# Optimization experiments

Hardware: AMD Instinct MI355X
Metric: run time of the kernel (lower is better)

Reference implementation:

```python
import jax, jax.numpy as jnp
import numpy as np

OUT = 7           # pooled output size
SR = 2            # sampling_ratio
SCALES = (0.25, 0.125, 0.0625, 0.03125)
K_MIN = 2         # -log2(scales[0])
CANON_SCALE = 224.0
CANON_LVL = 4.0
EPS = 1e-6


def map_levels(boxes):
    # boxes: [N,4] in image coords -> level index in [0, 3]
    area = (boxes[:, 2] - boxes[:, 0]) * (boxes[:, 3] - boxes[:, 1])
    s = jnp.sqrt(area)
    lvl = jnp.floor(CANON_LVL + jnp.log2(s / CANON_SCALE + EPS))
    lvl = jnp.clip(lvl, K_MIN, K_MIN + len(SCALES) - 1)
    return lvl.astype(jnp.int32) - K_MIN


def _sample_coords(lo, bin_sz):
    # sample points within each of OUT bins, SR samples per bin -> [OUT*SR]
    grid = (jnp.arange(OUT, dtype=jnp.float32)[:, None] * bin_sz
            + (jnp.arange(SR, dtype=jnp.float32)[None, :] + 0.5) * bin_sz / SR)
    return lo + grid.reshape(-1)


def _roi_align_single(feat, img, box, scale):
    # feat: [B,C,H,W] (closed over batch under vmap), img: scalar int, box: [4]
    H, W = feat.shape[2], feat.shape[3]
    x1 = box[0] * scale
    y1 = box[1] * scale
    x2 = box[2] * scale
    y2 = box[3] * scale
    roi_w = jnp.maximum(x2 - x1, 1.0)
    roi_h = jnp.maximum(y2 - y1, 1.0)
    ys = _sample_coords(y1, roi_h / OUT)  # [14]
    xs = _sample_coords(x1, roi_w / OUT)  # [14]
    P = OUT * SR
    yg = jnp.broadcast_to(ys[:, None], (P, P)).reshape(-1)  # [196]
    xg = jnp.broadcast_to(xs[None, :], (P, P)).reshape(-1)  # [196]
    # ROIAlign CUDA semantics: out-of-range samples contribute 0
    valid = (yg >= -1.0) & (yg <= H) & (xg >= -1.0) & (xg <= W)
    y = jnp.clip(yg, 0.0, H - 1)
    x = jnp.clip(xg, 0.0, W - 1)
    y0 = jnp.floor(y).astype(jnp.int32)
    x0 = jnp.floor(x).astype(jnp.int32)
    y1i = jnp.minimum(y0 + 1, H - 1)
    x1i = jnp.minimum(x0 + 1, W - 1)
    ly = y - y0
    lx = x - x0
    hy = 1.0 - ly
    hx = 1.0 - lx
    # advanced indices (img, y, x) separated by ':' slice -> result [196, C]
    v00 = feat[img, :, y0, x0]
    v01 = feat[img, :, y0, x1i]
    v10 = feat[img, :, y1i, x0]
    v11 = feat[img, :, y1i, x1i]
    val = ((hy * hx)[:, None] * v00 + (hy * lx)[:, None] * v01
           + (ly * hx)[:, None] * v10 + (ly * lx)[:, None] * v11)
    val = jnp.where(valid[:, None], val, 0.0)
    # [196,C] -> [OUT,SR,OUT,SR,C] -> average over sampling grid -> [OUT,OUT,C]
    val = val.reshape(OUT, SR, OUT, SR, -1).mean(axis=(1, 3))
    return jnp.transpose(val, (2, 0, 1))  # [C,7,7]


def _pooler(feats, boxes, img_ids):
    levels = map_levels(boxes)  # [N]
    N = boxes.shape[0]
    C = feats[0].shape[1]
    result = jnp.zeros((N, C, OUT, OUT), dtype=feats[0].dtype)
    roi_align = jax.vmap(_roi_align_single, in_axes=(None, 0, 0, None))
    for lvl, (feat, scale) in enumerate(zip(feats, SCALES)):
        out_l = roi_align(feat, img_ids, boxes, scale)  # [N,C,7,7]
        result = jnp.where((levels == lvl)[:, None, None, None], out_l, result)
    return result


def setup_inputs() -> dict:
    key = jax.random.key(0)
    ks = jax.random.split(key, 7)
    B, C, N = 2, 256, 1000
    feat0 = jax.random.normal(ks[0], (B, C, 200, 200), jnp.float32)
    feat1 = jax.random.normal(ks[1], (B, C, 100, 100), jnp.float32)
    feat2 = jax.random.normal(ks[2], (B, C, 50, 50), jnp.float32)
    feat3 = jax.random.normal(ks[3], (B, C, 25, 25), jnp.float32)
    # log-uniform box sizes in [16, 400] px spread ROIs across all 4 levels
    wh = jnp.exp(jax.random.uniform(ks[4], (N, 2), minval=jnp.log(16.0),
                                    maxval=jnp.log(400.0)))
    xy = jax.random.uniform(ks[5], (N, 2)) * (800.0 - wh)
    boxes = jnp.concatenate([xy, xy + wh], axis=1)  # [N,4] x1,y1,x2,y2
    img_ids = jax.random.randint(ks[6], (N,), 0, B, dtype=jnp.int32)
    return {"feat0": feat0, "feat1": feat1, "feat2": feat2, "feat3": feat3,
            "boxes": boxes, "img_ids": img_ids}


def reference(feat0, feat1, feat2, feat3, boxes, img_ids):
    return _pooler((feat0, feat1, feat2, feat3), boxes, img_ids)
```

## Files before the change

kernel.cpp:

```cpp
#include <hip/hip_runtime.h>
#include <hip/hip_fp16.h>

#define OUTD 7
#define PD 14
#define NCH 256

#define TOFF0 0
#define TOFF1 20480000
#define TOFF2 25600000
#define TOFF3 26880000
#define TTOT  27200000
#define TBASE_BYTES 16384

__global__ __launch_bounds__(1024)
void sort_kernel(const float* __restrict__ boxes,
                 const int*   __restrict__ img_ids,
                 int* __restrict__ order, int N)
{
    __shared__ unsigned long long kv[1024];
    const int t = threadIdx.x;

    unsigned int key = 0xFFFFFFFFu;
    if (t < N) {
        const float bx1 = boxes[t * 4 + 0];
        const float by1 = boxes[t * 4 + 1];
        const float bx2 = boxes[t * 4 + 2];
        const float by2 = boxes[t * 4 + 3];
        const float area = (bx2 - bx1) * (by2 - by1);
        const float s = sqrtf(area);
        float lvlf = floorf(4.0f + log2f(s / 224.0f + 1e-6f));
        lvlf = fminf(fmaxf(lvlf, 2.0f), 5.0f);
        const int lvl = (int)lvlf - 2;
        const float scales[4] = {0.25f, 0.125f, 0.0625f, 0.03125f};
        const float sc = scales[lvl];
        int cx = (int)(0.5f * (bx1 + bx2) * sc);
        int cy = (int)(0.5f * (by1 + by2) * sc);
        cx = min(max(cx, 0), 127);
        cy = min(max(cy, 0), 127);
        unsigned int m = 0;
#pragma unroll
        for (int b = 0; b < 7; ++b)
            m |= ((cy >> b) & 1u) << (2 * b + 1) | ((cx >> b) & 1u) << (2 * b);
        key = ((((unsigned)lvl << 1) | (unsigned)img_ids[t]) << 14) | m;
    }
    kv[t] = ((unsigned long long)key << 32) | (unsigned)t;
    __syncthreads();

    for (int k = 2; k <= 1024; k <<= 1) {
        for (int j = k >> 1; j > 0; j >>= 1) {
            const int ixj = t ^ j;
            if (ixj > t) {
                const bool up = ((t & k) == 0);
                const unsigned long long a = kv[t], b = kv[ixj];
                if ((a > b) == up) { kv[t] = b; kv[ixj] = a; }
            }
            __syncthreads();
        }
    }
    if (t < N) order[t] = (int)(kv[t] & 0xFFFFFFFFu);
}

__global__ __launch_bounds__(512)
void transpose_kernel(const float* __restrict__ f0, const float* __restrict__ f1,
                      const float* __restrict__ f2, const float* __restrict__ f3,
                      __half* __restrict__ T)
{
    const int t = threadIdx.x;
    int id = blockIdx.x;
    const int img = (id >= 832) ? 1 : 0; if (img) id -= 832;
    int lvl, pt;
    if (id < 625)      { lvl = 0; pt = id; }
    else if (id < 782) { lvl = 1; pt = id - 625; }
    else if (id < 822) { lvl = 2; pt = id - 782; }
    else               { lvl = 3; pt = id - 822; }

    const int  Ps[4]   = {40000, 10000, 2500, 625};
    const long TO[4]   = {TOFF0, TOFF1, TOFF2, TOFF3};
    const float* feats[4] = {f0, f1, f2, f3};
    const int P = Ps[lvl];
    const float* __restrict__ src = feats[lvl] + (size_t)img * NCH * (size_t)P;
    __half* __restrict__ dst = T + TO[lvl] + (size_t)img * (size_t)P * NCH;
    const int p0 = pt * 64;

    __shared__ float tile[64][260];

    const int a  = t & 15;
    const int cg = t >> 4;
    const int p4 = a * 4;

#pragma unroll
    for (int i = 0; i < 8; ++i) {
        const int cs = cg + 32 * i;
        const float* sp = src + (size_t)cs * P + p0;
        float4 v;
        if (((P & 3) == 0) && (p0 + p4 + 3 < P)) {
            v = *(const float4*)(sp + p4);
        } else {
            const int m = P - 1 - p0;
            v.x = sp[min(p4 + 0, m)]; v.y = sp[min(p4 + 1, m)];
            v.z = sp[min(p4 + 2, m)]; v.w = sp[min(p4 + 3, m)];
        }
        tile[p4 + 0][cs] = v.x;
        tile[p4 + 1][cs] = v.y;
        tile[p4 + 2][cs] = v.z;
        tile[p4 + 3][cs] = v.w;
    }
    __syncthreads();

    const int c4 = (t & 63) * 4;
    const int w  = t >> 6;
#pragma unroll
    for (int i = 0; i < 8; ++i) {
        const int p = w + 8 * i;
        if (p0 + p < P) {
            const __half2 h0 = __floats2half2_rn(tile[p][c4 + 0], tile[p][c4 + 1]);
            const __half2 h1 = __floats2half2_rn(tile[p][c4 + 2], tile[p][c4 + 3]);
            uint2 o;
            o.x = *(const unsigned int*)&h0;
            o.y = *(const unsigned int*)&h1;
            *(uint2*)(dst + (size_t)(p0 + p) * NCH + c4) = o;
        }
    }
}

__global__ __launch_bounds__(256)
void pooler_t_kernel(const __half* __restrict__ T,
                     const float* __restrict__ boxes,
                     const int*   __restrict__ img_ids,
                     const int*   __restrict__ order,
                     float* __restrict__ out, int N)
{
    int bx = blockIdx.x;
    int sidx;
    if ((N & 7) == 0) sidx = (bx & 7) * (N >> 3) + (bx >> 3);
    else              sidx = bx;
    const int roi = order[sidx];
    const int t = threadIdx.x;

    const float bx1 = boxes[roi * 4 + 0];
    const float by1 = boxes[roi * 4 + 1];
    const float bx2 = boxes[roi * 4 + 2];
    const float by2 = boxes[roi * 4 + 3];

    const float area = (bx2 - bx1) * (by2 - by1);
    const float s    = sqrtf(area);
    float lvlf = floorf(4.0f + log2f(s / 224.0f + 1e-6f));
    lvlf = fminf(fmaxf(lvlf, 2.0f), 5.0f);
    const int lvl = (int)lvlf - 2;

    const float scales[4] = {0.25f, 0.125f, 0.0625f, 0.03125f};
    const int   dims[4]   = {200, 100, 50, 25};
    const int   Ps[4]     = {40000, 10000, 2500, 625};
    const long  TO[4]     = {TOFF0, TOFF1, TOFF2, TOFF3};

    const float scale = scales[lvl];
    const int H = dims[lvl];
    const int W = H;
    const int img = img_ids[roi];
    const __half* __restrict__ tb = T + TO[lvl] + (size_t)img * (size_t)Ps[lvl] * NCH;

    const float x1 = bx1 * scale, y1 = by1 * scale;
    const float x2 = bx2 * scale, y2 = by2 * scale;
    const float roi_w = fmaxf(x2 - x1, 1.0f);
    const float roi_h = fmaxf(y2 - y1, 1.0f);
    const float bw = roi_w / (float)OUTD;
    const float bh = roi_h / (float)OUTD;

    __shared__ float4 s_yt[PD];
    __shared__ float4 s_xt[PD];
    __shared__ float  s_out[49 * 260];

    if (t < PD) {
        const int i = t >> 1, j = t & 1;
        const float yg = y1 + (float)i * bh + ((float)j + 0.5f) * bh * 0.5f;
        const float v = ((yg >= -1.0f) && (yg <= (float)H)) ? 1.0f : 0.0f;
        const float y = fminf(fmaxf(yg, 0.0f), (float)(H - 1));
        const int y0 = (int)floorf(y);
        const int y1i = min(y0 + 1, H - 1);
        const float ly = y - (float)y0;
        float4 r;
        r.x = __int_as_float(y0 * W);
        r.y = __int_as_float(y1i * W);
        r.z = (1.0f - ly) * v;
        r.w = ly * v;
        s_yt[t] = r;
    } else if (t < 2 * PD) {
        const int tt = t - PD;
        const int i = tt >> 1, j = tt & 1;
        const float xg = x1 + (float)i * bw + ((float)j + 0.5f) * bw * 0.5f;
        const float v = ((xg >= -1.0f) && (xg <= (float)W)) ? 1.0f : 0.0f;
        const float x = fminf(fmaxf(xg, 0.0f), (float)(W - 1));
        const int x0 = (int)floorf(x);
        const int x1i = min(x0 + 1, W - 1);
        const float lx = x - (float)x0;
        float4 r;
        r.x = __int_as_float(x0);
        r.y = __int_as_float(x1i);
        r.z = (1.0f - lx) * v;
        r.w = lx * v;
        s_xt[tt] = r;
    }
    __syncthreads();

    const int lane = t & 63;
    const int w    = t >> 6;
    const int c4   = lane * 4;

    for (int bin = w; bin < 49; bin += 4) {
        const int ph = (bin * 37) >> 8;
        const int pw = bin - ph * 7;
        float4 acc = {0.0f, 0.0f, 0.0f, 0.0f};
#pragma unroll
        for (int sy = 0; sy < 2; ++sy) {
            const float4 yt = s_yt[ph * 2 + sy];
            const int r0 = __float_as_int(yt.x);
            const int r1 = __float_as_int(yt.y);
            const float hy = yt.z, ly = yt.w;
#pragma unroll
            for (int sx = 0; sx < 2; ++sx) {
                const float4 xt = s_xt[pw * 2 + sx];
                const int xa = __float_as_int(xt.x);
                const int xb = __float_as_int(xt.y);
                const float hx = xt.z, lx = xt.w;
                const float w00 = hy * hx, w01 = hy * lx, w10 = ly * hx, w11 = ly * lx;

                const uint2 q00 = *(const uint2*)(tb + ((size_t)(r0 + xa) << 8) + c4);
                const uint2 q01 = *(const uint2*)(tb + ((size_t)(r0 + xb) << 8) + c4);
                const uint2 q10 = *(const uint2*)(tb + ((size_t)(r1 + xa) << 8) + c4);
                const uint2 q11 = *(const uint2*)(tb + ((size_t)(r1 + xb) << 8) + c4);

                const float2 a0 = __half22float2(*(const __half2*)&q00.x);
                const float2 a1 = __half22float2(*(const __half2*)&q00.y);
                const float2 b0 = __half22float2(*(const __half2*)&q01.x);
                const float2 b1 = __half22float2(*(const __half2*)&q01.y);
                const float2 c0 = __half22float2(*(const __half2*)&q10.x);
                const float2 c1 = __half22float2(*(const __half2*)&q10.y);
                const float2 d0 = __half22float2(*(const __half2*)&q11.x);
                const float2 d1 = __half22float2(*(const __half2*)&q11.y);

                acc.x += w00 * a0.x + w01 * b0.x + w10 * c0.x + w11 * d0.x;
                acc.y += w00 * a0.y + w01 * b0.y + w10 * c0.y + w11 * d0.y;
                acc.z += w00 * a1.x + w01 * b1.x + w10 * c1.x + w11 * d1.x;
                acc.w += w00 * a1.y + w01 * b1.y + w10 * c1.y + w11 * d1.y;
            }
        }
        float4 r;
        r.x = acc.x * 0.25f; r.y = acc.y * 0.25f;
        r.z = acc.z * 0.25f; r.w = acc.w * 0.25f;
        *(float4*)(&s_out[bin * 260 + c4]) = r;
    }
    __syncthreads();

    float* __restrict__ outbase = out + (size_t)roi * (NCH * 49);
#pragma unroll
    for (int i = 0; i < 49; ++i) {
        const int e = t + i * 256;
        const int c = (int)(((unsigned)e * 21400u) >> 20);
        const int bin = e - c * 49;
        outbase[e] = s_out[bin * 260 + c];
    }
}

#define LCHUNK 32
__global__ __launch_bounds__(256)
void pooler_legacy(const float* __restrict__ f0,
                   const float* __restrict__ f1,
                   const float* __restrict__ f2,
                   const float* __restrict__ f3,
                   const float* __restrict__ boxes,
                   const int*   __restrict__ img_ids,
                   const int*   __restrict__ order,
                   float* __restrict__ out, int N)
{
    int bx = blockIdx.x;
    int sidx;
    if ((N & 7) == 0) sidx = (bx & 7) * (N >> 3) + (bx >> 3);
    else              sidx = bx;
    const int roi = order[sidx];

    const int c0  = blockIdx.y * LCHUNK;
    const int t   = threadIdx.x;

    const float bx1 = boxes[roi * 4 + 0];
    const float by1 = boxes[roi * 4 + 1];
    const float bx2 = boxes[roi * 4 + 2];
    const float by2 = boxes[roi * 4 + 3];

    const float area = (bx2 - bx1) * (by2 - by1);
    const float s    = sqrtf(area);
    float lvlf = floorf(4.0f + log2f(s / 224.0f + 1e-6f));
    lvlf = fminf(fmaxf(lvlf, 2.0f), 5.0f);
    const int lvl = (int)lvlf - 2;

    const float scales[4] = {0.25f, 0.125f, 0.0625f, 0.03125f};
    const int   dims[4]   = {200, 100, 50, 25};
    const float* feats[4] = {f0, f1, f2, f3};

    const float scale = scales[lvl];
    const int H = dims[lvl];
    const int W = H;
    const int plane = H * W;

    const int img = img_ids[roi];
    const float* __restrict__ base0 =
        feats[lvl] + (size_t)img * NCH * (size_t)plane + (size_t)c0 * plane;

    const float x1 = bx1 * scale, y1 = by1 * scale;
    const float x2 = bx2 * scale, y2 = by2 * scale;
    const float roi_w = fmaxf(x2 - x1, 1.0f);
    const float roi_h = fmaxf(y2 - y1, 1.0f);
    const float bw = roi_w / (float)OUTD;
    const float bh = roi_h / (float)OUTD;

    __shared__ float4 s_yt[PD];
    __shared__ float4 s_xt[PD];
    __shared__ float4 s_xw[OUTD];
    __shared__ int    s_xf[OUTD];
    __shared__ int    s_ok[OUTD];

    if (t < PD) {
        const int i = t >> 1, j = t & 1;
        const float yg = y1 + (float)i * bh + ((float)j + 0.5f) * bh * 0.5f;
        const float v = ((yg >= -1.0f) && (yg <= (float)H)) ? 1.0f : 0.0f;
        const float y = fminf(fmaxf(yg, 0.0f), (float)(H - 1));
        const int y0 = (int)floorf(y);
        const int y1i = min(y0 + 1, H - 1);
        const float ly = y - (float)y0;
        float4 r;
        r.x = __int_as_float(y0 * W);
        r.y = __int_as_float(y1i * W);
        r.z = (1.0f - ly) * v;
        r.w = ly * v;
        s_yt[t] = r;
    } else if (t < 2 * PD) {
        const int tt = t - PD;
        const int i = tt >> 1, j = tt & 1;
        const float xg = x1 + (float)i * bw + ((float)j + 0.5f) * bw * 0.5f;
        const float v = ((xg >= -1.0f) && (xg <= (float)W)) ? 1.0f : 0.0f;
        const float x = fminf(fmaxf(xg, 0.0f), (float)(W - 1));
        const int x0 = (int)floorf(x);
        const float lx = x - (float)x0;
        const float hx = 1.0f - lx;
        const int edge = (x0 == W - 1);
        float4 r;
        r.x = __int_as_float(min(x0, W - 2));
        r.y = edge ? 0.0f   : hx * v;
        r.z = edge ? hx * v : lx * v;
        r.w = 0.0f;
        s_xt[tt] = r;
    } else if (t < 2 * PD + OUTD) {
        const int pw = t - 2 * PD;
        float w[4] = {0.0f, 0.0f, 0.0f, 0.0f};
        int ca[2], cb[2];
        float hxv[2], lxv[2];
#pragma unroll
        for (int j = 0; j < 2; ++j) {
            const float xg = x1 + (float)pw * bw + ((float)j + 0.5f) * bw * 0.5f;
            const float v = ((xg >= -1.0f) && (xg <= (float)W)) ? 1.0f : 0.0f;
            const float x = fminf(fmaxf(xg, 0.0f), (float)(W - 1));
            const int x0 = (int)floorf(x);
            const float lx = x - (float)x0;
            ca[j] = x0;
            cb[j] = min(x0 + 1, W - 1);
            hxv[j] = (1.0f - lx) * v;
            lxv[j] = lx * v;
        }
        const int ok = (cb[1] - ca[0]) <= 3;
        int xf = min(ca[0], W - 4);
        if (xf < 0) xf = 0;
        w[(ca[0] - xf) & 3] += hxv[0];
        w[(cb[0] - xf) & 3] += lxv[0];
        w[(ca[1] - xf) & 3] += hxv[1];
        w[(cb[1] - xf) & 3] += lxv[1];
        float4 wv; wv.x = w[0]; wv.y = w[1]; wv.z = w[2]; wv.w = w[3];
        s_xw[pw] = wv;
        s_xf[pw] = xf;
        s_ok[pw] = ok;
    }
    __syncthreads();

    const bool fused = s_ok[0] && s_ok[1] && s_ok[2] && s_ok[3] &&
                       s_ok[4] && s_ok[5] && s_ok[6];

    float* __restrict__ outbase = out + ((size_t)roi * NCH + c0) * 49;

    if (fused) {
        auto g4 = [&](const float* __restrict__ fp, int ph, int pw, float4* P) {
            const float4 yt0 = s_yt[2 * ph];
            const float4 yt1 = s_yt[2 * ph + 1];
            const int xf = s_xf[pw];
            P[0] = *(const float4*)(fp + __float_as_int(yt0.x) + xf);
            P[1] = *(const float4*)(fp + __float_as_int(yt0.y) + xf);
            P[2] = *(const float4*)(fp + __float_as_int(yt1.x) + xf);
            P[3] = *(const float4*)(fp + __float_as_int(yt1.y) + xf);
        };
        auto r4 = [&](int ph, int pw, const float4* P) -> float {
            const float4 w   = s_xw[pw];
            const float4 yt0 = s_yt[2 * ph];
            const float4 yt1 = s_yt[2 * ph + 1];
            const float d0 = w.x * P[0].x + w.y * P[0].y + w.z * P[0].z + w.w * P[0].w;
            const float d1 = w.x * P[1].x + w.y * P[1].y + w.z * P[1].z + w.w * P[1].w;
            const float d2 = w.x * P[2].x + w.y * P[2].y + w.z * P[2].z + w.w * P[2].w;
            const float d3 = w.x * P[3].x + w.y * P[3].y + w.z * P[3].z + w.w * P[3].w;
            return yt0.z * d0 + yt0.w * d1 + yt1.z * d2 + yt1.w * d3;
        };
        {
            int eA[4], phA[4], pwA[4];
            const float* fpA[4];
#pragma unroll
            for (int j = 0; j < 4; ++j) {
                const int e = t + j * 256;
                const int c = e / 49, bin = e - c * 49;
                phA[j] = bin / 7;
                pwA[j] = bin - phA[j] * 7;
                eA[j]  = e;
                fpA[j] = base0 + (size_t)c * plane;
            }
            float4 P[4][4];
#pragma unroll
            for (int j = 0; j < 4; ++j) g4(fpA[j], phA[j], pwA[j], P[j]);
            __builtin_amdgcn_sched_barrier(0);
#pragma unroll
            for (int j = 0; j < 4; ++j)
                outbase[eA[j]] = r4(phA[j], pwA[j], P[j]) * 0.25f;
        }
        {
            int eA[2], phA[2], pwA[2];
            const float* fpA[2];
#pragma unroll
            for (int j = 0; j < 2; ++j) {
                const int e = t + (4 + j) * 256;
                const int c = e / 49, bin = e - c * 49;
                phA[j] = bin / 7;
                pwA[j] = bin - phA[j] * 7;
                eA[j]  = e;
                fpA[j] = base0 + (size_t)c * plane;
            }
            float4 P[2][4];
#pragma unroll
            for (int j = 0; j < 2; ++j) g4(fpA[j], phA[j], pwA[j], P[j]);
            __builtin_amdgcn_sched_barrier(0);
#pragma unroll
            for (int j = 0; j < 2; ++j)
                outbase[eA[j]] = r4(phA[j], pwA[j], P[j]) * 0.25f;
        }
        if (t < 32) {
            const int e = 1536 + t;
            const int c = e / 49, bin = e - c * 49;
            const int ph = bin / 7, pw = bin - ph * 7;
            const float* fp = base0 + (size_t)c * plane;
            float4 P[4];
            g4(fp, ph, pw, P);
            outbase[e] = r4(ph, pw, P) * 0.25f;
        }
    } else {
        auto gather = [&](const float* __restrict__ fp, int ph, int pw, float2* P) {
#pragma unroll
            for (int sy = 0; sy < 2; ++sy) {
                const float4 yt = s_yt[ph * 2 + sy];
                const int ro0 = __float_as_int(yt.x);
                const int ro1 = __float_as_int(yt.y);
#pragma unroll
                for (int sx = 0; sx < 2; ++sx) {
                    const float4 xt = s_xt[pw * 2 + sx];
                    const int xa = __float_as_int(xt.x);
                    P[(sy * 2 + sx) * 2 + 0] = *(const float2*)(fp + ro0 + xa);
                    P[(sy * 2 + sx) * 2 + 1] = *(const float2*)(fp + ro1 + xa);
                }
            }
        };
        auto reduce = [&](int ph, int pw, const float2* P) -> float {
            float acc = 0.0f;
#pragma unroll
            for (int sy = 0; sy < 2; ++sy) {
                const float4 yt = s_yt[ph * 2 + sy];
                const float hy = yt.z, ly = yt.w;
#pragma unroll
                for (int sx = 0; sx < 2; ++sx) {
                    const float4 xt = s_xt[pw * 2 + sx];
                    const float wlo = xt.y, whi = xt.z;
                    const float2 p0 = P[(sy * 2 + sx) * 2 + 0];
                    const float2 p1 = P[(sy * 2 + sx) * 2 + 1];
                    acc += hy * (wlo * p0.x + whi * p0.y)
                         + ly * (wlo * p1.x + whi * p1.y);
                }
            }
            return acc;
        };
#pragma unroll
        for (int kk = 0; kk < 2; ++kk) {
            int eA[3], phA[3], pwA[3];
            const float* fpA[3];
#pragma unroll
            for (int j = 0; j < 3; ++j) {
                const int e = t + (kk * 3 + j) * 256;
                const int c = e / 49, bin = e - c * 49;
                phA[j] = bin / 7;
                pwA[j] = bin - phA[j] * 7;
                eA[j]  = e;
                fpA[j] = base0 + (size_t)c * plane;
            }
            float2 P[3][8];
#pragma unroll
            for (int j = 0; j < 3; ++j) gather(fpA[j], phA[j], pwA[j], P[j]);
            __builtin_amdgcn_sched_barrier(0);
#pragma unroll
            for (int j = 0; j < 3; ++j)
                outbase[eA[j]] = reduce(phA[j], pwA[j], P[j]) * 0.25f;
        }
        if (t < 32) {
            const int e = 1536 + t;
            const int c = e / 49, bin = e - c * 49;
            const int ph = bin / 7, pw = bin - ph * 7;
            const float* fp = base0 + (size_t)c * plane;
            float2 P[8];
            gather(fp, ph, pw, P);
            outbase[e] = reduce(ph, pw, P) * 0.25f;
        }
    }
}

extern "C" void kernel_launch(void* const* d_in, const int* in_sizes, int n_in,
                              void* d_out, int out_size, void* d_ws, size_t ws_size,
                              hipStream_t stream) {
    const float* f0    = (const float*)d_in[0];
    const float* f1    = (const float*)d_in[1];
    const float* f2    = (const float*)d_in[2];
    const float* f3    = (const float*)d_in[3];
    const float* boxes = (const float*)d_in[4];
    const int*   ids   = (const int*)d_in[5];
    float* out = (float*)d_out;
    int*   order = (int*)d_ws;

    const int N = in_sizes[4] / 4;

    const size_t need = (size_t)TBASE_BYTES + (size_t)TTOT * sizeof(__half);

    sort_kernel<<<1, 1024, 0, stream>>>(boxes, ids, order, N);

    if (ws_size >= need) {
        __half* T = (__half*)((char*)d_ws + TBASE_BYTES);
        transpose_kernel<<<1664, 512, 0, stream>>>(f0, f1, f2, f3, T);
        pooler_t_kernel<<<N, 256, 0, stream>>>(T, boxes, ids, order, out, N);
    } else {
        dim3 grid(N, NCH / LCHUNK);
        pooler_legacy<<<grid, 256, 0, stream>>>(f0, f1, f2, f3, boxes, ids, order, out, N);
    }
}
```

Measured before the change: 217.6 us.

## Fuse ROI sort into transpose kernel and halve transpose tile size

The separate single-block sort launch is folded into the transpose kernel as an extra block, so the sort runs alongside the feature transpose instead of as its own serialized launch. The transpose tile shrinks from 64 to 32 positions with 256-thread blocks, doubling the block count and cutting shared memory per block, which is meant to raise occupancy. The sort block now handles 1024 elements with 256 threads in strided loops. The fast path is limited to N of at most 1024.

After: 232.2 us. 1.07x slower.

```diff
diff --git a/kernel.cpp b/kernel.cpp
--- a/kernel.cpp
+++ b/kernel.cpp
@@ -12,20 +12,18 @@
 #define TTOT  27200000
 #define TBASE_BYTES 16384
 
-__global__ __launch_bounds__(1024)
-void sort_kernel(const float* __restrict__ boxes,
-                 const int*   __restrict__ img_ids,
-                 int* __restrict__ order, int N)
+#define NTILES_IMG 1662
+#define NB_TRANS   3324
+
+__device__ __forceinline__ unsigned int roi_key(const float* boxes,
+                                                const int* img_ids, int e, int N)
 {
-    __shared__ unsigned long long kv[1024];
-    const int t = threadIdx.x;
-
     unsigned int key = 0xFFFFFFFFu;
-    if (t < N) {
-        const float bx1 = boxes[t * 4 + 0];
-        const float by1 = boxes[t * 4 + 1];
-        const float bx2 = boxes[t * 4 + 2];
-        const float by2 = boxes[t * 4 + 3];
+    if (e < N) {
+        const float bx1 = boxes[e * 4 + 0];
+        const float by1 = boxes[e * 4 + 1];
+        const float bx2 = boxes[e * 4 + 2];
+        const float by2 = boxes[e * 4 + 3];
         const float area = (bx2 - bx1) * (by2 - by1);
         const float s = sqrtf(area);
         float lvlf = floorf(4.0f + log2f(s / 224.0f + 1e-6f));
@@ -41,38 +39,53 @@
 #pragma unroll
         for (int b = 0; b < 7; ++b)
             m |= ((cy >> b) & 1u) << (2 * b + 1) | ((cx >> b) & 1u) << (2 * b);
-        key = ((((unsigned)lvl << 1) | (unsigned)img_ids[t]) << 14) | m;
-    }
-    kv[t] = ((unsigned long long)key << 32) | (unsigned)t;
-    __syncthreads();
-
-    for (int k = 2; k <= 1024; k <<= 1) {
-        for (int j = k >> 1; j > 0; j >>= 1) {
-            const int ixj = t ^ j;
-            if (ixj > t) {
-                const bool up = ((t & k) == 0);
-                const unsigned long long a = kv[t], b = kv[ixj];
-                if ((a > b) == up) { kv[t] = b; kv[ixj] = a; }
-            }
-            __syncthreads();
-        }
-    }
-    if (t < N) order[t] = (int)(kv[t] & 0xFFFFFFFFu);
+        key = ((((unsigned)lvl << 1) | (unsigned)img_ids[e]) << 14) | m;
+    }
+    return key;
 }
 
-__global__ __launch_bounds__(512)
-void transpose_kernel(const float* __restrict__ f0, const float* __restrict__ f1,
-                      const float* __restrict__ f2, const float* __restrict__ f3,
-                      __half* __restrict__ T)
+__global__ __launch_bounds__(256)
+void prep_kernel(const float* __restrict__ f0, const float* __restrict__ f1,
+                 const float* __restrict__ f2, const float* __restrict__ f3,
+                 const float* __restrict__ boxes,
+                 const int*   __restrict__ img_ids,
+                 int* __restrict__ order,
+                 __half* __restrict__ T, int N)
 {
+    __shared__ __align__(16) float smbuf[32 * 260];
     const int t = threadIdx.x;
+
+    if (blockIdx.x == NB_TRANS) {
+        unsigned long long* kv = (unsigned long long*)smbuf;
+        for (int e = t; e < 1024; e += 256)
+            kv[e] = ((unsigned long long)roi_key(boxes, img_ids, e, N) << 32)
+                    | (unsigned)e;
+        __syncthreads();
+        for (int k = 2; k <= 1024; k <<= 1) {
+            for (int j = k >> 1; j > 0; j >>= 1) {
+                for (int i = t; i < 1024; i += 256) {
+                    const int ixj = i ^ j;
+                    if (ixj > i) {
+                        const bool up = ((i & k) == 0);
+                        const unsigned long long a = kv[i], b = kv[ixj];
+                        if ((a > b) == up) { kv[i] = b; kv[ixj] = a; }
+                    }
+                }
+                __syncthreads();
+            }
+        }
+        for (int e = t; e < 1024; e += 256)
+            if (e < N) order[e] = (int)(kv[e] & 0xFFFFFFFFu);
+        return;
+    }
+
     int id = blockIdx.x;
-    const int img = (id >= 832) ? 1 : 0; if (img) id -= 832;
+    const int img = (id >= NTILES_IMG) ? 1 : 0; if (img) id -= NTILES_IMG;
     int lvl, pt;
-    if (id < 625)      { lvl = 0; pt = id; }
-    else if (id < 782) { lvl = 1; pt = id - 625; }
-    else if (id < 822) { lvl = 2; pt = id - 782; }
-    else               { lvl = 3; pt = id - 822; }
+    if (id < 1250)      { lvl = 0; pt = id; }
+    else if (id < 1563) { lvl = 1; pt = id - 1250; }
+    else if (id < 1642) { lvl = 2; pt = id - 1563; }
+    else                { lvl = 3; pt = id - 1642; }
 
     const int  Ps[4]   = {40000, 10000, 2500, 625};
     const long TO[4]   = {TOFF0, TOFF1, TOFF2, TOFF3};
@@ -80,17 +93,17 @@
     const int P = Ps[lvl];
     const float* __restrict__ src = feats[lvl] + (size_t)img * NCH * (size_t)P;
     __half* __restrict__ dst = T + TO[lvl] + (size_t)img * (size_t)P * NCH;
-    const int p0 = pt * 64;
-
-    __shared__ float tile[64][260];
-
-    const int a  = t & 15;
-    const int cg = t >> 4;
-    const int p4 = a * 4;
+    const int p0 = pt * 32;
+
+    float (*tile)[260] = (float (*)[260])smbuf;
+
+    const int a   = t & 7;
+    const int cg0 = t >> 3;
+    const int p4  = a * 4;
 
 #pragma unroll
     for (int i = 0; i < 8; ++i) {
-        const int cs = cg + 32 * i;
+        const int cs = cg0 + 32 * i;
         const float* sp = src + (size_t)cs * P + p0;
         float4 v;
         if (((P & 3) == 0) && (p0 + p4 + 3 < P)) {
@@ -111,7 +124,7 @@
     const int w  = t >> 6;
 #pragma unroll
     for (int i = 0; i < 8; ++i) {
-        const int p = w + 8 * i;
+        const int p = w + 4 * i;
         if (p0 + p < P) {
             const __half2 h0 = __floats2half2_rn(tile[p][c4 + 0], tile[p][c4 + 1]);
             const __half2 h1 = __floats2half2_rn(tile[p][c4 + 2], tile[p][c4 + 3]);
@@ -259,6 +272,29 @@
         const int bin = e - c * 49;
         outbase[e] = s_out[bin * 260 + c];
     }
+}
+
+__global__ __launch_bounds__(1024)
+void sort_kernel(const float* __restrict__ boxes,
+                 const int*   __restrict__ img_ids,
+                 int* __restrict__ order, int N)
+{
+    __shared__ unsigned long long kv[1024];
+    const int t = threadIdx.x;
+    kv[t] = ((unsigned long long)roi_key(boxes, img_ids, t, N) << 32) | (unsigned)t;
+    __syncthreads();
+    for (int k = 2; k <= 1024; k <<= 1) {
+        for (int j = k >> 1; j > 0; j >>= 1) {
+            const int ixj = t ^ j;
+            if (ixj > t) {
+                const bool up = ((t & k) == 0);
+                const unsigned long long a = kv[t], b = kv[ixj];
+                if ((a > b) == up) { kv[t] = b; kv[ixj] = a; }
+            }
+            __syncthreads();
+        }
+    }
+    if (t < N) order[t] = (int)(kv[t] & 0xFFFFFFFFu);
 }
 
 #define LCHUNK 32
@@ -536,13 +572,13 @@
 
     const size_t need = (size_t)TBASE_BYTES + (size_t)TTOT * sizeof(__half);
 
-    sort_kernel<<<1, 1024, 0, stream>>>(boxes, ids, order, N);
-
-    if (ws_size >= need) {
+    if (ws_size >= need && N <= 1024) {
         __half* T = (__half*)((char*)d_ws + TBASE_BYTES);
-        transpose_kernel<<<1664, 512, 0, stream>>>(f0, f1, f2, f3, T);
+        prep_kernel<<<NB_TRANS + 1, 256, 0, stream>>>(f0, f1, f2, f3,
+                                                      boxes, ids, order, T, N);
         pooler_t_kernel<<<N, 256, 0, stream>>>(T, boxes, ids, order, out, N);
     } else {
+        sort_kernel<<<1, 1024, 0, stream>>>(boxes, ids, order, N);
         dim3 grid(N, NCH / LCHUNK);
         pooler_legacy<<<grid, 256, 0, stream>>>(f0, f1, f2, f3, boxes, ids, order, out, N);
     }
```
